# Kernel optimization log

Measured on AMD Instinct MI355X. Metric: run time of the kernel, lower is better.

## Reference

```python
import jax, jax.numpy as jnp
import numpy as np
from jax.scipy.special import erf

SIGMA = 1.0
TWOPI = 2.0 * np.pi
NORM_FACTOR = 90.0474


def setup_inputs() -> dict:
    key = jax.random.key(0)
    k1, k2 = jax.random.split(key)
    N = 6144
    q = jax.random.normal(k1, (N, 1), dtype=jnp.float32)
    r = jax.random.normal(k2, (N, 3), dtype=jnp.float32)
    cell = jnp.zeros((1, 3, 3), dtype=jnp.float32)  # det=0 -> realspace branch
    return {"q": q, "r": r, "cell": cell}


def reference(q, r, cell):
    # Realspace Ewald (non-periodic branch): sum_{i != j} q_i q_j erf(d_ij/(sigma*sqrt(2)))/d_ij
    # (cell has det < 1e-6, so the torch module takes compute_potential_realspace;
    #  batch=None -> a single system)
    n = r.shape[0]
    diff = r[:, None, :] - r[None, :, :]            # [N, N, 3]
    d2 = jnp.sum(diff * diff, axis=-1)              # [N, N]
    eye = jnp.eye(n, dtype=bool)
    d2_safe = jnp.where(eye, 1.0, d2)               # avoid 0 on diagonal
    dist = jnp.sqrt(d2_safe)
    w = erf(dist / (SIGMA * jnp.sqrt(2.0))) / dist  # erf(d/(sigma*sqrt2)) / d
    w = jnp.where(eye, 0.0, w)                      # remove self-interaction (diag)
    # pot = sum_{i!=j, c} q_ic q_jc w_ij
    pot = jnp.einsum('ic,jc,ij->', q, q, w)
    pot = pot / TWOPI / 2.0 * NORM_FACTOR
    # torch: stack over batches -> [1,1], sum(dim=1) -> [1]
    return jnp.reshape(pot, (1,))
```

## Files before the change

### kernel.cpp

```cpp
#include <hip/hip_runtime.h>
#include <math.h>


#if __has_builtin(__builtin_amdgcn_rsqf)
#define FRSQ(x) __builtin_amdgcn_rsqf(x)
#else
#define FRSQ(x) rsqrtf(x)
#endif
#if __has_builtin(__builtin_amdgcn_rcpf)
#define FRCP(x) __builtin_amdgcn_rcpf(x)
#else
#define FRCP(x) (1.0f / (x))
#endif

#define B1 0.19685360f
#define B2 0.11519450f
#define B3 0.00034366f
#define B4 0.01952700f

template <bool CHECK>
__device__ __forceinline__ void pair_body(const float4 v, int jj, int i,
                                          float xi, float yi, float zi,
                                          float& acc) {
  float dx = xi - v.x;
  float dy = yi - v.y;
  float dz = zi - v.z;
  float d2 = fmaf(dx, dx, fmaf(dy, dy, dz * dz));
  float qk = v.w;
  if (CHECK) {
    bool take = (jj > i);
    d2 = take ? d2 : 1.0f;
    qk = take ? qk : 0.0f;
  }
  float rinv = FRSQ(d2);
  float d = d2 * rinv;
  float poly = fmaf(fmaf(fmaf(B4, d, B3), d, B2), d, B1);
  poly = fmaf(poly, d, 1.0f);
  float y = FRCP(poly);
  float y2 = y * y;
  float y4 = y2 * y2;
  float w = fmaf(-y4, rinv, rinv);
  acc = fmaf(qk, w, acc);
}

template <bool CHECK>
__device__ __forceinline__ float tile_sum(const float4* __restrict__ tile,
                                          int cnt, int jbeg, int i, float xi,
                                          float yi, float zi) {
  float acc0 = 0.f, acc1 = 0.f;
  int k = 0;
#pragma unroll 8
  for (; k + 2 <= cnt; k += 2) {
    pair_body<CHECK>(tile[k], jbeg + k, i, xi, yi, zi, acc0);
    pair_body<CHECK>(tile[k + 1], jbeg + k + 1, i, xi, yi, zi, acc1);
  }
  if (k < cnt) pair_body<CHECK>(tile[k], jbeg + k, i, xi, yi, zi, acc0);
  return acc0 + acc1;
}

__global__ __launch_bounds__(256) void ewald_tri(
    const float* __restrict__ q, const float* __restrict__ r,
    float* __restrict__ partial, int n) {
  const int tid = threadIdx.x;
  const int bid = blockIdx.x;
  const int jslices = (n + 63) >> 6;

  int ib = 0, cum = 0;
  while (true) {
    int c = jslices - 4 * ib;
    if (c <= 0 || cum + c > bid) break;
    cum += c;
    ++ib;
  }
  const int js = 4 * ib + (bid - cum);

  const int ibeg = ib << 8;
  const int jbeg = js << 6;
  const int jend = min(jbeg + 64, n);
  const bool pure_above = (jbeg >= ibeg + 256);

  __shared__ float4 tile[64];
  if (tid < 64) {
    int j = jbeg + tid;
    if (j < n) tile[tid] = make_float4(r[3 * j], r[3 * j + 1], r[3 * j + 2], q[j]);
  }

  const int i = ibeg + tid;
  float qi = 0.f, xi = 0.f, yi = 0.f, zi = 0.f;
  if (i < n) {
    qi = q[i];
    xi = r[3 * i];
    yi = r[3 * i + 1];
    zi = r[3 * i + 2];
  }
  __syncthreads();

  const int cnt = jend - jbeg;
  float acc;
  if (pure_above)
    acc = tile_sum<false>(tile, cnt, jbeg, i, xi, yi, zi);
  else
    acc = tile_sum<true>(tile, cnt, jbeg, i, xi, yi, zi);
  acc *= qi;

  for (int m = 32; m > 0; m >>= 1) acc += __shfl_xor(acc, m, 64);
  __shared__ float wsum[4];
  const int lane = tid & 63;
  const int wid = tid >> 6;
  if (lane == 0) wsum[wid] = acc;
  __syncthreads();
  if (tid == 0)
    partial[bid] = (wsum[0] + wsum[1]) + (wsum[2] + wsum[3]);
}

__global__ __launch_bounds__(1024) void reduce_partials(
    const float* __restrict__ partial, float* __restrict__ out, int np,
    float scale) {
  const int tid = threadIdx.x;
  float acc = 0.f;
  for (int idx = tid; idx < np; idx += 1024) acc += partial[idx];
  for (int m = 32; m > 0; m >>= 1) acc += __shfl_xor(acc, m, 64);
  __shared__ float wsum[16];
  const int lane = tid & 63;
  const int wid = tid >> 6;
  if (lane == 0) wsum[wid] = acc;
  __syncthreads();
  if (tid == 0) {
    float s = 0.f;
    for (int w = 0; w < 16; ++w) s += wsum[w];
    out[0] = s * scale;
  }
}

extern "C" void kernel_launch(void* const* d_in, const int* in_sizes, int n_in,
                              void* d_out, int out_size, void* d_ws,
                              size_t ws_size, hipStream_t stream) {
  const float* q = (const float*)d_in[0];
  const float* r = (const float*)d_in[1];
  const int n = in_sizes[0];
  float* out = (float*)d_out;
  float* partial = (float*)d_ws;

  const int iblocks = (n + 255) / 256;
  const int jslices = (n + 63) / 64;
  int nblocks = 0;
  for (int ib = 0; ib < iblocks; ++ib) {
    int c = jslices - 4 * ib;
    if (c > 0) nblocks += c;
  }

  ewald_tri<<<nblocks, 256, 0, stream>>>(q, r, partial, n);

  const float scale = (float)(90.0474 / (2.0 * M_PI));
  reduce_partials<<<1, 1024, 0, stream>>>(partial, out, nblocks, scale);
}
```

Measured before the change: 18.82 us.

## Remap triangular work to per-warp 64x64 tiles with closed-form tile index

Each warp now owns an independent 64x64 upper-triangular tile, so masked work is confined to diagonal tiles and block-wide barriers are removed. Tile coordinates come from a sqrt-based inversion of the triangular index instead of a loop. Out-of-range entries are padded with far-away coordinates and zero charge, so no count check is needed. This trades more partial sums for the reduce kernel against less wasted pair work near the diagonal.

```diff
diff --git a/kernel.cpp b/kernel.cpp
--- a/kernel.cpp
+++ b/kernel.cpp
@@ -19,7 +19,7 @@
 #define B4 0.01952700f
 
 template <bool CHECK>
-__device__ __forceinline__ void pair_body(const float4 v, int jj, int i,
+__device__ __forceinline__ void pair_body(const float4 v, int k, int lane,
                                           float xi, float yi, float zi,
                                           float& acc) {
   float dx = xi - v.x;
@@ -28,7 +28,7 @@
   float d2 = fmaf(dx, dx, fmaf(dy, dy, dz * dz));
   float qk = v.w;
   if (CHECK) {
-    bool take = (jj > i);
+    bool take = (k > lane);
     d2 = take ? d2 : 1.0f;
     qk = take ? qk : 0.0f;
   }
@@ -45,72 +45,65 @@
 
 template <bool CHECK>
 __device__ __forceinline__ float tile_sum(const float4* __restrict__ tile,
-                                          int cnt, int jbeg, int i, float xi,
-                                          float yi, float zi) {
+                                          int lane, float xi, float yi,
+                                          float zi) {
   float acc0 = 0.f, acc1 = 0.f;
-  int k = 0;
 #pragma unroll 8
-  for (; k + 2 <= cnt; k += 2) {
-    pair_body<CHECK>(tile[k], jbeg + k, i, xi, yi, zi, acc0);
-    pair_body<CHECK>(tile[k + 1], jbeg + k + 1, i, xi, yi, zi, acc1);
+  for (int k = 0; k < 64; k += 2) {
+    pair_body<CHECK>(tile[k], k, lane, xi, yi, zi, acc0);
+    pair_body<CHECK>(tile[k + 1], k + 1, lane, xi, yi, zi, acc1);
   }
-  if (k < cnt) pair_body<CHECK>(tile[k], jbeg + k, i, xi, yi, zi, acc0);
   return acc0 + acc1;
 }
 
 __global__ __launch_bounds__(256) void ewald_tri(
     const float* __restrict__ q, const float* __restrict__ r,
-    float* __restrict__ partial, int n) {
+    float* __restrict__ partial, int n, int nt, int ntiles) {
   const int tid = threadIdx.x;
-  const int bid = blockIdx.x;
-  const int jslices = (n + 63) >> 6;
+  const int lane = tid & 63;
+  const int wid = tid >> 6;
+  const int g = blockIdx.x * 4 + wid;
+  if (g >= ntiles) return;
 
-  int ib = 0, cum = 0;
-  while (true) {
-    int c = jslices - 4 * ib;
-    if (c <= 0 || cum + c > bid) break;
-    cum += c;
-    ++ib;
-  }
-  const int js = 4 * ib + (bid - cum);
+  const float a = (float)nt + 0.5f;
+  int ti = (int)(a - sqrtf(fmaf(a, a, -2.0f * (float)g)));
+  if (ti < 0) ti = 0;
+  if (ti >= nt) ti = nt - 1;
+#define CUM(t) ((t) * nt - ((t) * ((t)-1)) / 2)
+  while (CUM(ti + 1) <= g) ++ti;
+  while (CUM(ti) > g) --ti;
+  const int tj = ti + (g - CUM(ti));
+#undef CUM
 
-  const int ibeg = ib << 8;
-  const int jbeg = js << 6;
-  const int jend = min(jbeg + 64, n);
-  const bool pure_above = (jbeg >= ibeg + 256);
+  const int ibeg = ti << 6;
+  const int jbeg = tj << 6;
 
-  __shared__ float4 tile[64];
-  if (tid < 64) {
-    int j = jbeg + tid;
-    if (j < n) tile[tid] = make_float4(r[3 * j], r[3 * j + 1], r[3 * j + 2], q[j]);
+  __shared__ float4 tile[4][64];
+  {
+    int j = jbeg + lane;
+    float4 v = make_float4(1e10f, 1e10f, 1e10f, 0.f);
+    if (j < n) v = make_float4(r[3 * j], r[3 * j + 1], r[3 * j + 2], q[j]);
+    tile[wid][lane] = v;
   }
 
-  const int i = ibeg + tid;
-  float qi = 0.f, xi = 0.f, yi = 0.f, zi = 0.f;
+  const int i = ibeg + lane;
+  float qi = 0.f, xi = 1e10f, yi = 1e10f, zi = 1e10f;
   if (i < n) {
     qi = q[i];
     xi = r[3 * i];
     yi = r[3 * i + 1];
     zi = r[3 * i + 2];
   }
-  __syncthreads();
 
-  const int cnt = jend - jbeg;
   float acc;
-  if (pure_above)
-    acc = tile_sum<false>(tile, cnt, jbeg, i, xi, yi, zi);
+  if (ti == tj)
+    acc = tile_sum<true>(tile[wid], lane, xi, yi, zi);
   else
-    acc = tile_sum<true>(tile, cnt, jbeg, i, xi, yi, zi);
+    acc = tile_sum<false>(tile[wid], lane, xi, yi, zi);
   acc *= qi;
 
   for (int m = 32; m > 0; m >>= 1) acc += __shfl_xor(acc, m, 64);
-  __shared__ float wsum[4];
-  const int lane = tid & 63;
-  const int wid = tid >> 6;
-  if (lane == 0) wsum[wid] = acc;
-  __syncthreads();
-  if (tid == 0)
-    partial[bid] = (wsum[0] + wsum[1]) + (wsum[2] + wsum[3]);
+  if (lane == 0) partial[g] = acc;
 }
 
 __global__ __launch_bounds__(1024) void reduce_partials(
@@ -141,16 +134,12 @@
   float* out = (float*)d_out;
   float* partial = (float*)d_ws;
 
-  const int iblocks = (n + 255) / 256;
-  const int jslices = (n + 63) / 64;
-  int nblocks = 0;
-  for (int ib = 0; ib < iblocks; ++ib) {
-    int c = jslices - 4 * ib;
-    if (c > 0) nblocks += c;
-  }
+  const int nt = (n + 63) / 64;
+  const int ntiles = nt * (nt + 1) / 2;
+  const int nblocks = (ntiles + 3) / 4;
 
-  ewald_tri<<<nblocks, 256, 0, stream>>>(q, r, partial, n);
+  ewald_tri<<<nblocks, 256, 0, stream>>>(q, r, partial, n, nt, ntiles);
 
   const float scale = (float)(90.0474 / (2.0 * M_PI));
-  reduce_partials<<<1, 1024, 0, stream>>>(partial, out, nblocks, scale);
+  reduce_partials<<<1, 1024, 0, stream>>>(partial, out, ntiles, scale);
 }
```

Result: slower. 19.20 us (+2.0%).
